# Kernel optimization log

Measured on AMD Instinct MI355X. Metric: run time of the kernel, lower is better.

## Reference

```python
import jax, jax.numpy as jnp
from jax import lax
import numpy as np

# Straight-through-estimator sign (standard BNN binarization):
# fwd: sign(x) with sign(0)=+1; bwd: pass gradient where |x|<=1 (hardtanh STE).
@jax.custom_vjp
def sign_ste(x):
    return jnp.where(x >= 0, 1.0, -1.0).astype(x.dtype)

def _sign_fwd(x):
    return sign_ste(x), x

def _sign_bwd(x, g):
    return (g * (jnp.abs(x) <= 1.0).astype(g.dtype),)

sign_ste.defvjp(_sign_fwd, _sign_bwd)

EPS = 1e-5  # BatchNorm eps (torch default)

def bn4(x, g, b):  # BatchNorm2d, training-mode batch stats, x: [N,C,H,W]
    m = x.mean((0, 2, 3), keepdims=True)
    v = x.var((0, 2, 3), keepdims=True)
    return g[None, :, None, None] * (x - m) * lax.rsqrt(v + EPS) + b[None, :, None, None]

def bn1(x, g, b):  # BatchNorm1d, x: [N,C]
    m = x.mean(0, keepdims=True)
    v = x.var(0, keepdims=True)
    return g * (x - m) * lax.rsqrt(v + EPS) + b

def bconv(x, W, b, first):
    # BinarizedConv2d: binarize weights always; binarize input except first layer.
    xb = x if first else sign_ste(x)
    y = lax.conv_general_dilated(xb, sign_ste(W), (1, 1), [(1, 1), (1, 1)],
                                 dimension_numbers=('NCHW', 'OIHW', 'NCHW'))
    return y + b[None, :, None, None]

def maxpool2(x):
    return lax.reduce_window(x, -jnp.inf, lax.max, (1, 1, 2, 2), (1, 1, 2, 2), 'VALID')

def ht(x):  # Hardtanh
    return jnp.clip(x, -1.0, 1.0)

CONV_CH = [(3, 64), (64, 128), (128, 256), (256, 256), (256, 512), (512, 512), (512, 512), (512, 512)]
LIN_CH = [(512, 512), (512, 512), (512, 10)]
POOL_AFTER = (0, 1, 3, 5, 7)  # conv indices followed by MaxPool2d

def setup_inputs():
    key = jax.random.key(0)
    ks = iter(jax.random.split(key, 64))
    d = {"x": jax.random.normal(next(ks), (256, 3, 32, 32), jnp.float32)}
    for i, (ci, co) in enumerate(CONV_CH):
        d[f"cw{i}"] = jax.random.normal(next(ks), (co, ci, 3, 3), jnp.float32) * 0.1
        d[f"cb{i}"] = jnp.zeros((co,), jnp.float32)
        d[f"cg{i}"] = jnp.ones((co,), jnp.float32)
        d[f"ct{i}"] = jnp.zeros((co,), jnp.float32)
    for i, (ci, co) in enumerate(LIN_CH):
        d[f"lw{i}"] = jax.random.normal(next(ks), (co, ci), jnp.float32) * 0.1
        d[f"lb{i}"] = jnp.zeros((co,), jnp.float32)
        d[f"lg{i}"] = jnp.ones((co,), jnp.float32)
        d[f"lt{i}"] = jnp.zeros((co,), jnp.float32)
    return d

def _forward(x, cw, cb, cg, ct, lw, lb, lg, lt):
    h = x
    for i in range(8):
        h = bconv(h, cw[i], cb[i], i == 0)
        if i in POOL_AFTER:
            h = maxpool2(h)
        h = ht(bn4(h, cg[i], ct[i]))
    h = h.reshape(h.shape[0], -1)  # [N, 512] after 5 pools on 32x32
    for i in range(3):
        h = sign_ste(h) @ sign_ste(lw[i]).T + lb[i]  # BinarizedLinear
        h = bn1(h, lg[i], lt[i])
        if i < 2:
            h = ht(h)  # Dropout is identity in eval mode
    return jax.nn.log_softmax(h, axis=-1)

def reference(x,
              cw0, cb0, cg0, ct0, cw1, cb1, cg1, ct1, cw2, cb2, cg2, ct2,
              cw3, cb3, cg3, ct3, cw4, cb4, cg4, ct4, cw5, cb5, cg5, ct5,
              cw6, cb6, cg6, ct6, cw7, cb7, cg7, ct7,
              lw0, lb0, lg0, lt0, lw1, lb1, lg1, lt1, lw2, lb2, lg2, lt2):
    cw = [cw0, cw1, cw2, cw3, cw4, cw5, cw6, cw7]
    cb = [cb0, cb1, cb2, cb3, cb4, cb5, cb6, cb7]
    cg = [cg0, cg1, cg2, cg3, cg4, cg5, cg6, cg7]
    ct = [ct0, ct1, ct2, ct3, ct4, ct5, ct6, ct7]
    lw = [lw0, lw1, lw2]
    lb = [lb0, lb1, lb2]
    lg = [lg0, lg1, lg2]
    lt = [lt0, lt1, lt2]
    return _forward(x, cw, cb, cg, ct, lw, lb, lg, lt)
```

## Files before the change

### kernel.cpp

```cpp
#include <hip/hip_runtime.h>
#include <hip/hip_bf16.h>

typedef unsigned long long u64;

#define EPSV 1e-5

__device__ __forceinline__ int imax(int a, int b) { return a > b ? a : b; }
__device__ __forceinline__ int iclamp(int v, int lo, int hi) { return v < lo ? lo : (v > hi ? hi : v); }

struct PrepArgs {
    const float* src[10];
    u64* dst[10];
    int CW[10];
    int Co[10];
    int taps[10];
    int rowbase[11];
    u64* accs;
    int naccs;
};

__global__ __launch_bounds__(256) void prep_kernel(PrepArgs a) {
    __shared__ float buf[4608];
    const int blk = blockIdx.x;
    int z = blk * 19 + threadIdx.x;
    if (threadIdx.x < 19 && z < a.naccs) a.accs[z] = 0ULL;

    int l = 0;
    while (l < 9 && blk >= a.rowbase[l + 1]) ++l;
    const int row = blk - a.rowbase[l];
    const int CW = a.CW[l];
    const int taps = a.taps[l];
    const int nf = CW * 64 * taps;
    const float* srow = a.src[l] + (size_t)row * nf;
    for (int i = threadIdx.x; i < nf; i += 256) buf[i] = srow[i];
    __syncthreads();
    const int t = threadIdx.x;
    if (t < taps * CW) {
        u64 bits = 0;
        if (taps == 9) {
            int k = t % 9, w = t / 9;
            for (int j = 0; j < 64; ++j) bits |= (u64)(buf[(w * 64 + j) * 9 + k] >= 0.f) << j;
            a.dst[l][(size_t)(k * CW + w) * a.Co[l] + row] = bits;
        } else {
            for (int j = 0; j < 64; ++j) bits |= (u64)(buf[t * 64 + j] >= 0.f) << j;
            a.dst[l][(size_t)row * CW + t] = bits;
        }
    }
}

__global__ __launch_bounds__(256) void conv0_lane(const float* __restrict__ x,
                                                  const float* __restrict__ wgt,
                                                  float* __restrict__ out,
                                                  double* __restrict__ dacc) {
    const int lane = threadIdx.x & 63;
    const int wave = threadIdx.x >> 6;
    float ws[27];
#pragma unroll
    for (int j = 0; j < 27; ++j) ws[j] = (wgt[lane * 27 + j] >= 0.f) ? 1.f : -1.f;

    const int gp0 = blockIdx.x * 32;
    const int n = gp0 >> 8;
    const int ypA = (gp0 >> 4) & 15;
    const int yb = 2 * ypA - 1;

    __shared__ float simg[3][6][34];
    const float* xb = x + (size_t)n * 3072;
    for (int t = threadIdx.x; t < 612; t += 256) {
        int ci = t / 204;
        int rem = t % 204;
        int r = rem / 34;
        int cc = rem % 34;
        int yy = yb + r;
        int xx = cc - 1;
        float v = 0.f;
        if ((unsigned)yy < 32u && (unsigned)xx < 32u) v = xb[(ci * 32 + yy) * 32 + xx];
        simg[ci][r][cc] = v;
    }
    __syncthreads();

    double s1 = 0.0, s2 = 0.0;
#pragma unroll 2
    for (int pi = 0; pi < 8; ++pi) {
        const int lp = wave * 8 + pi;
        const int gp = gp0 + lp;
        const int xp = lp & 15;
        const int rbase = 2 * (lp >> 4);
        const int cbase = 2 * xp;
        float win[3][4][4];
#pragma unroll
        for (int ci = 0; ci < 3; ++ci)
#pragma unroll
            for (int r = 0; r < 4; ++r)
#pragma unroll
                for (int c = 0; c < 4; ++c) win[ci][r][c] = simg[ci][rbase + r][cbase + c];
        float a00 = 0.f, a01 = 0.f, a10 = 0.f, a11 = 0.f;
#pragma unroll
        for (int ci = 0; ci < 3; ++ci)
#pragma unroll
            for (int ky = 0; ky < 3; ++ky)
#pragma unroll
                for (int kx = 0; kx < 3; ++kx) {
                    float wv = ws[ci * 9 + ky * 3 + kx];
                    a00 += win[ci][ky][kx] * wv;
                    a01 += win[ci][ky][kx + 1] * wv;
                    a10 += win[ci][ky + 1][kx] * wv;
                    a11 += win[ci][ky + 1][kx + 1] * wv;
                }
        float val = fmaxf(fmaxf(a00, a01), fmaxf(a10, a11));
        out[(size_t)gp * 64 + lane] = val;
        s1 += (double)val;
        s2 += (double)val * (double)val;
    }
    __shared__ double sh1[4][64], sh2[4][64];
    sh1[wave][lane] = s1;
    sh2[wave][lane] = s2;
    __syncthreads();
    if (threadIdx.x < 64) {
        double t1 = 0.0, t2 = 0.0;
#pragma unroll
        for (int r = 0; r < 4; ++r) { t1 += sh1[r][threadIdx.x]; t2 += sh2[r][threadIdx.x]; }
        double* sh = dacc + (size_t)(blockIdx.x & 7) * 1024;
        atomicAdd(&sh[2 * threadIdx.x], t1);
        atomicAdd(&sh[2 * threadIdx.x + 1], t2);
    }
}

__global__ __launch_bounds__(256) void bnpack_f(const float* __restrict__ in,
                                                const double* __restrict__ dacc,
                                                const float* __restrict__ g,
                                                const float* __restrict__ b,
                                                u64* __restrict__ act, int count) {
    __shared__ float2 sthr[64];
    if (threadIdx.x < 64) {
        int i = threadIdx.x;
        double S1 = 0.0, S2 = 0.0;
#pragma unroll
        for (int s = 0; s < 8; ++s) {
            S1 += dacc[s * 1024 + 2 * i];
            S2 += dacc[s * 1024 + 2 * i + 1];
        }
        double m = S1 / count;
        double var = S2 / count - m * m;
        double sc = (double)g[i] / sqrt(var + EPSV);
        float2 r;
        if (sc == 0.0) r = make_float2(b[i] >= 0.f ? -3.0e38f : 3.0e38f, 1.f);
        else {
            double t = m - (double)b[i] / sc;
            r = make_float2((float)t, sc > 0.0 ? 1.f : -1.f);
        }
        sthr[i] = r;
    }
    __syncthreads();
    int tid = blockIdx.x * 256 + threadIdx.x;
    int part = tid & 3;
    int word = tid >> 2;
    const float4* r4 = (const float4*)(in + (size_t)word * 64 + part * 16);
    u64 bits = 0;
#pragma unroll
    for (int q = 0; q < 4; ++q) {
        float4 v = r4[q];
        float vv[4] = {v.x, v.y, v.z, v.w};
#pragma unroll
        for (int u = 0; u < 4; ++u) {
            int c = part * 16 + q * 4 + u;
            float2 t = sthr[c];
            bool bit = (t.y > 0.f) ? (vv[u] >= t.x) : (vv[u] <= t.x);
            bits |= (u64)bit << c;
        }
    }
    bits |= __shfl_xor(bits, 1);
    bits |= __shfl_xor(bits, 2);
    if (part == 0) act[word] = bits;
}

__global__ __launch_bounds__(256) void bnpack_i(const short* __restrict__ in,
                                                const u64* __restrict__ iacc,
                                                const float* __restrict__ g,
                                                const float* __restrict__ b,
                                                u64* __restrict__ act, int Co, int wshift,
                                                int count) {
    __shared__ int2 sthr[520];
    for (int i = threadIdx.x; i < Co; i += 256) {
        long long S1 = 0, S2 = 0;
#pragma unroll
        for (int s = 0; s < 8; ++s) {
            S1 += (long long)iacc[s * 1024 + 2 * i];
            S2 += (long long)iacc[s * 1024 + 2 * i + 1];
        }
        double m = (double)S1 / count;
        double var = (double)S2 / count - m * m;
        double sc = (double)g[i] / sqrt(var + EPSV);
        int2 r;
        if (sc == 0.0) r = make_int2(b[i] >= 0.f ? (int)0x80000000 : 0x7fffffff, 0);
        else {
            double t = m - (double)b[i] / sc;
            if (t > 1.0e9) t = 1.0e9;
            if (t < -1.0e9) t = -1.0e9;
            r = (sc > 0.0) ? make_int2((int)ceil(t), 0) : make_int2((int)floor(t), 1);
        }
        sthr[(i >> 6) * 65 + (i & 63)] = r;
    }
    __syncthreads();
    int tid = blockIdx.x * 256 + threadIdx.x;
    int part = tid & 3;
    int word = tid >> 2;
    int w = word & ((1 << wshift) - 1);
    int pix = word >> wshift;
    const int4* r4 = (const int4*)(in + (size_t)pix * Co + (w << 6) + part * 16);
    u64 bits = 0;
#pragma unroll
    for (int q = 0; q < 2; ++q) {
        int4 v = r4[q];
        int words4[4] = {v.x, v.y, v.z, v.w};
#pragma unroll
        for (int u = 0; u < 4; ++u) {
#pragma unroll
            for (int h = 0; h < 2; ++h) {
                int c = part * 16 + q * 8 + u * 2 + h;
                int val = (int)(short)((h == 0) ? (words4[u] & 0xffff) : ((unsigned)words4[u] >> 16));
                int2 t = sthr[w * 65 + c];
                bool bit = t.y ? (val <= t.x) : (val >= t.x);
                bits |= (u64)bit << c;
            }
        }
    }
    bits |= __shfl_xor(bits, 1);
    bits |= __shfl_xor(bits, 2);
    if (part == 0) act[word] = bits;
}

template <int CW, int HIN, bool POOL, int WC, bool INTERIOR>
__device__ __forceinline__ void row_accum(const u64* __restrict__ inb,
                                          const u64* __restrict__ wpkT, int Co, int co,
                                          const int* yoff, const bool* ry, int* cnt) {
    constexpr int HP = POOL ? HIN / 2 : HIN;
    constexpr int WS = POOL ? 4 : 3;
    constexpr int NA = POOL ? 4 : 1;
#pragma unroll 1
    for (int w0 = 0; w0 < CW; w0 += WC) {
        u64 wg[9 * WC];
#pragma unroll
        for (int k = 0; k < 9; ++k)
#pragma unroll
            for (int w = 0; w < WC; ++w)
                wg[k * WC + w] = wpkT[(size_t)(k * CW + w0 + w) * Co + co];
        u64 cur[WS][WS][WC];
#pragma unroll
        for (int d = 0; d < WS; ++d) {
            int cc = d - 1;
            int ccc = cc < 0 ? 0 : cc;
#pragma unroll
            for (int r = 0; r < WS; ++r) {
                const u64* p = inb + yoff[r] + ccc * CW + w0;
                if (WC == 1) {
                    cur[r][d][0] = p[0];
                } else {
                    ulonglong2 v = *(const ulonglong2*)p;
                    cur[r][d][0] = v.x;
                    cur[r][d][1] = v.y;
                }
            }
        }
#pragma unroll
        for (int xp = 0; xp < HP; ++xp) {
            if constexpr (POOL) {
#pragma unroll
                for (int py = 0; py < 2; ++py)
#pragma unroll
                    for (int qx = 0; qx < 2; ++qx)
#pragma unroll
                        for (int ky = 0; ky < 3; ++ky)
#pragma unroll
                            for (int kx = 0; kx < 3; ++kx) {
                                int d = qx + kx;
                                int cc = 2 * xp + d - 1;
                                if (cc >= 0 && cc < HIN) {
#pragma unroll
                                    for (int w = 0; w < WC; ++w) {
                                        int pc = (int)__popcll(cur[py + ky][d][w] ^
                                                               wg[(ky * 3 + kx) * WC + w]);
                                        if constexpr (INTERIOR)
                                            cnt[xp * NA + py * 2 + qx] += pc;
                                        else
                                            cnt[xp * NA + py * 2 + qx] += ry[py + ky] ? pc : 0;
                                    }
                                }
                            }
            } else {
#pragma unroll
                for (int ky = 0; ky < 3; ++ky)
#pragma unroll
                    for (int kx = 0; kx < 3; ++kx) {
                        int cc = xp + kx - 1;
                        if (cc >= 0 && cc < HIN) {
#pragma unroll
                            for (int w = 0; w < WC; ++w) {
                                int pc = (int)__popcll(cur[ky][kx][w] ^
                                                       wg[(ky * 3 + kx) * WC + w]);
                                if constexpr (INTERIOR)
                                    cnt[xp] += pc;
                                else
                                    cnt[xp] += ry[ky] ? pc : 0;
                            }
                        }
                    }
            }
            if (xp < HP - 1) {
                if constexpr (POOL) {
#pragma unroll
                    for (int r = 0; r < WS; ++r)
#pragma unroll
                        for (int w = 0; w < WC; ++w) {
                            cur[r][0][w] = cur[r][2][w];
                            cur[r][1][w] = cur[r][3][w];
                        }
#pragma unroll
                    for (int dd = 2; dd < 4; ++dd) {
                        int cc = 2 * (xp + 1) + dd - 1;
                        int ccc = cc >= HIN ? HIN - 1 : cc;
#pragma unroll
                        for (int r = 0; r < WS; ++r) {
                            const u64* p = inb + yoff[r] + ccc * CW + w0;
                            if (WC == 1) {
                                cur[r][dd][0] = p[0];
                            } else {
                                ulonglong2 v = *(const ulonglong2*)p;
                                cur[r][dd][0] = v.x;
                                cur[r][dd][1] = v.y;
                            }
                        }
                    }
                } else {
#pragma unroll
                    for (int r = 0; r < WS; ++r)
#pragma unroll
                        for (int w = 0; w < WC; ++w) {
                            cur[r][0][w] = cur[r][1][w];
                            cur[r][1][w] = cur[r][2][w];
                        }
                    int cc = xp + 2;
                    int ccc = cc >= HIN ? HIN - 1 : cc;
#pragma unroll
                    for (int r = 0; r < WS; ++r) {
                        const u64* p = inb + yoff[r] + ccc * CW + w0;
                        if (WC == 1) {
                            cur[r][2][0] = p[0];
                        } else {
                            ulonglong2 v = *(const ulonglong2*)p;
                            cur[r][2][0] = v.x;
                            cur[r][2][1] = v.y;
                        }
                    }
                }
            }
        }
    }
}

template <int CW, int HIN, bool POOL, int WC>
__global__ __launch_bounds__(256) void bconv_row(const u64* __restrict__ in,
                                                 const u64* __restrict__ wpkT,
                                                 short* __restrict__ out,
                                                 u64* __restrict__ iacc, int Co) {
    constexpr int HP = POOL ? HIN / 2 : HIN;
    constexpr int WS = POOL ? 4 : 3;
    constexpr int NA = POOL ? 4 : 1;
    const int lane = threadIdx.x & 63;
    const int co = blockIdx.y * 64 + lane;
    const int grow = blockIdx.x * 4 + (threadIdx.x >> 6);
    const int n = grow / HP;
    const int yp = grow % HP;
    const int y0 = (POOL ? 2 * yp : yp) - 1;
    const u64* inb = in + (size_t)n * (HIN * HIN * CW);
    int yoff[WS];
    bool ry[WS];
#pragma unroll
    for (int r = 0; r < WS; ++r) {
        int y = y0 + r;
        ry[r] = (unsigned)y < (unsigned)HIN;
        int yc = iclamp(y, 0, HIN - 1);
        yoff[r] = yc * HIN * CW;
    }
    int cnt[HP * NA];
#pragma unroll
    for (int i = 0; i < HP * NA; ++i) cnt[i] = 0;

    if (yp > 0 && yp < HP - 1)
        row_accum<CW, HIN, POOL, WC, true>(inb, wpkT, Co, co, yoff, ry, cnt);
    else
        row_accum<CW, HIN, POOL, WC, false>(inb, wpkT, Co, co, yoff, ry, cnt);

    const int nr0 = (int)ry[0] + (int)ry[1] + (int)ry[2];
    const int nr1 = POOL ? ((int)ry[1] + (int)ry[2] + (int)ry[WS - 1]) : 0;

    int s1 = 0;
    long long s2 = 0;
    short* orow = out + (size_t)grow * HP * Co + co;
#pragma unroll
    for (int xp = 0; xp < HP; ++xp) {
        int ival;
        if constexpr (POOL) {
            int best = -2147483647;
#pragma unroll
            for (int py = 0; py < 2; ++py) {
                const int nrv = py ? nr1 : nr0;
#pragma unroll
                for (int qx = 0; qx < 2; ++qx) {
                    int ncols = 3;
                    if (xp == 0 && qx == 0) ncols = 2;
                    if (xp == HP - 1 && qx == 1) ncols = 2;
                    int v = 64 * CW * nrv * ncols - 2 * cnt[xp * NA + py * 2 + qx];
                    best = imax(best, v);
                }
            }
            ival = best;
        } else {
            const int ncols = (xp == 0 || xp == HIN - 1) ? 2 : 3;
            ival = 64 * CW * nr0 * ncols - 2 * cnt[xp];
        }
        orow[(size_t)xp * Co] = (short)ival;
        s1 += ival;
        s2 += (long long)ival * ival;
    }

    __shared__ u64 sacc[128];
    if (threadIdx.x < 128) sacc[threadIdx.x] = 0ULL;
    __syncthreads();
    atomicAdd(&sacc[lane], (u64)(long long)s1);
    atomicAdd(&sacc[64 + lane], (u64)s2);
    __syncthreads();
    u64* sh = iacc + (size_t)(blockIdx.x & 7) * 1024;
    if (threadIdx.x < 64)
        atomicAdd(&sh[2 * (blockIdx.y * 64 + threadIdx.x)], sacc[threadIdx.x]);
    else if (threadIdx.x < 128)
        atomicAdd(&sh[2 * (blockIdx.y * 64 + threadIdx.x - 64) + 1], sacc[threadIdx.x]);
}

template <int CW, int HIN, bool POOL>
__global__ __launch_bounds__(256) void bconv_tiny(const u64* __restrict__ in,
                                                  const u64* __restrict__ wpkT,
                                                  short* __restrict__ out,
                                                  u64* __restrict__ iacc, int Co) {
    constexpr int NPX = HIN * HIN;
    constexpr int HP = POOL ? HIN / 2 : HIN;
    const int lane = threadIdx.x & 63;
    const int co = blockIdx.y * 64 + lane;
    const int n = blockIdx.x * 4 + (threadIdx.x >> 6);
    const u64* inb = in + (size_t)n * CW * NPX;
    int cnt[NPX];
#pragma unroll
    for (int i = 0; i < NPX; ++i) cnt[i] = 0;

#pragma unroll 2
    for (int w = 0; w < CW; ++w) {
        u64 win[NPX];
#pragma unroll
        for (int i = 0; i < NPX; ++i) win[i] = inb[i * CW + w];
#pragma unroll
        for (int k = 0; k < 9; ++k) {
            u64 wb = wpkT[(size_t)(k * CW + w) * Co + co];
            const int ky = k / 3, kx = k % 3;
#pragma unroll
            for (int py = 0; py < HIN; ++py)
#pragma unroll
                for (int px = 0; px < HIN; ++px) {
                    const int yy = py + ky - 1, xx = px + kx - 1;
                    if (yy >= 0 && yy < HIN && xx >= 0 && xx < HIN)
                        cnt[py * HIN + px] += (int)__popcll(win[yy * HIN + xx] ^ wb);
                }
        }
    }

    int fin[NPX];
#pragma unroll
    for (int py = 0; py < HIN; ++py)
#pragma unroll
        for (int px = 0; px < HIN; ++px) {
            const int nk = ((py == 0 || py == HIN - 1) ? 2 : 3) *
                           ((px == 0 || px == HIN - 1) ? 2 : 3);
            fin[py * HIN + px] = 64 * CW * nk - 2 * cnt[py * HIN + px];
        }

    short vals[HP * HP];
    if constexpr (POOL) {
#pragma unroll
        for (int py = 0; py < HP; ++py)
#pragma unroll
            for (int px = 0; px < HP; ++px)
                vals[py * HP + px] = (short)imax(
                    imax(fin[(2 * py) * HIN + 2 * px], fin[(2 * py) * HIN + 2 * px + 1]),
                    imax(fin[(2 * py + 1) * HIN + 2 * px], fin[(2 * py + 1) * HIN + 2 * px + 1]));
    } else {
#pragma unroll
        for (int i = 0; i < NPX; ++i) vals[i] = (short)fin[i];
    }
#pragma unroll
    for (int p = 0; p < HP * HP; ++p) out[(size_t)(n * HP * HP + p) * Co + co] = vals[p];

    long long s1 = 0, s2 = 0;
#pragma unroll
    for (int p = 0; p < HP * HP; ++p) {
        s1 += vals[p];
        s2 += (long long)vals[p] * vals[p];
    }
    __shared__ u64 sacc[128];
    if (threadIdx.x < 128) sacc[threadIdx.x] = 0ULL;
    __syncthreads();
    atomicAdd(&sacc[lane], (u64)s1);
    atomicAdd(&sacc[64 + lane], (u64)s2);
    __syncthreads();
    u64* sh = iacc + (size_t)(blockIdx.x & 7) * 1024;
    if (threadIdx.x < 64)
        atomicAdd(&sh[2 * (blockIdx.y * 64 + threadIdx.x)], sacc[threadIdx.x]);
    else if (threadIdx.x < 128)
        atomicAdd(&sh[2 * (blockIdx.y * 64 + threadIdx.x - 64) + 1], sacc[threadIdx.x]);
}

__global__ __launch_bounds__(256) void lin_kernel(const u64* __restrict__ hp,
                                                  const u64* __restrict__ wp,
                                                  const float* __restrict__ lb,
                                                  const float* __restrict__ g,
                                                  const float* __restrict__ bta,
                                                  u64* __restrict__ op) {
    int o = blockIdx.x;
    int n = threadIdx.x;
    const u64* hr = hp + n * 8;
    const u64* wr = wp + o * 8;
    int s = 0;
#pragma unroll
    for (int w = 0; w < 8; ++w) s += (int)__popcll(hr[w] ^ wr[w]);
    float val = (float)(512 - 2 * s) + lb[o];
    __shared__ double sh1[256], sh2[256];
    sh1[n] = (double)val;
    sh2[n] = (double)val * (double)val;
    __syncthreads();
    for (int st = 128; st > 0; st >>= 1) {
        if (n < st) {
            sh1[n] += sh1[n + st];
            sh2[n] += sh2[n + st];
        }
        __syncthreads();
    }
    __shared__ float sm, siv;
    if (n == 0) {
        double m = sh1[0] / 256.0;
        double var = sh2[0] / 256.0 - m * m;
        sm = (float)m;
        siv = (float)(1.0 / sqrt(var + EPSV));
    }
    __syncthreads();
    float zz = g[o] * (val - sm) * siv + bta[o];
    if (zz >= 0.f) atomicOr(&op[(size_t)n * 8 + (o >> 6)], 1ULL << (o & 63));
}

__global__ __launch_bounds__(256) void lin2_lsm(const u64* __restrict__ hp,
                                                const u64* __restrict__ wp,
                                                const float* __restrict__ lb,
                                                const float* __restrict__ g,
                                                const float* __restrict__ bta,
                                                float* __restrict__ out) {
    const int n = threadIdx.x;
    const int lane = n & 63;
    const int wave = n >> 6;
    u64 h[8];
#pragma unroll
    for (int w = 0; w < 8; ++w) h[w] = hp[n * 8 + w];
    float v[10];
#pragma unroll
    for (int o = 0; o < 10; ++o) {
        int s = 0;
#pragma unroll
        for (int w = 0; w < 8; ++w) s += (int)__popcll(h[w] ^ wp[o * 8 + w]);
        v[o] = (float)(512 - 2 * s) + lb[o];
    }
    __shared__ double w1[4][10], w2[4][10];
#pragma unroll
    for (int o = 0; o < 10; ++o) {
        double a = (double)v[o];
        double b = a * a;
#pragma unroll
        for (int off = 32; off > 0; off >>= 1) {
            a += __shfl_xor(a, off);
            b += __shfl_xor(b, off);
        }
        if (lane == 0) {
            w1[wave][o] = a;
            w2[wave][o] = b;
        }
    }
    __syncthreads();
    float z[10];
#pragma unroll
    for (int o = 0; o < 10; ++o) {
        double S1 = w1[0][o] + w1[1][o] + w1[2][o] + w1[3][o];
        double S2 = w2[0][o] + w2[1][o] + w2[2][o] + w2[3][o];
        double m = S1 / 256.0;
        double var = S2 / 256.0 - m * m;
        float sm = (float)m;
        float siv = (float)(1.0 / sqrt(var + EPSV));
        z[o] = g[o] * (v[o] - sm) * siv + bta[o];
    }
    float mx = z[0];
#pragma unroll
    for (int o = 1; o < 10; ++o) mx = fmaxf(mx, z[o]);
    float se = 0.f;
#pragma unroll
    for (int o = 0; o < 10; ++o) se += expf(z[o] - mx);
    float ls = logf(se);
#pragma unroll
    for (int o = 0; o < 10; ++o) out[n * 10 + o] = z[o] - mx - ls;
}

extern "C" void kernel_launch(void* const* d_in, const int* in_sizes, int n_in, void* d_out,
                              int out_size, void* d_ws, size_t ws_size, hipStream_t stream) {
    (void)in_sizes; (void)n_in; (void)out_size; (void)ws_size;
    const float* x = (const float*)d_in[0];
    const float *cw[8], *cb[8], *cg[8], *ct[8];
    for (int i = 0; i < 8; ++i) {
        cw[i] = (const float*)d_in[1 + 4 * i];
        cb[i] = (const float*)d_in[2 + 4 * i];
        cg[i] = (const float*)d_in[3 + 4 * i];
        ct[i] = (const float*)d_in[4 + 4 * i];
    }
    const float *lw[3], *lb[3], *lg[3], *lt[3];
    for (int i = 0; i < 3; ++i) {
        lw[i] = (const float*)d_in[33 + 4 * i];
        lb[i] = (const float*)d_in[34 + 4 * i];
        lg[i] = (const float*)d_in[35 + 4 * i];
        lt[i] = (const float*)d_in[36 + 4 * i];
    }

    static const int CIs[8] = {3, 64, 128, 256, 256, 512, 512, 512};
    static const int COs[8] = {64, 128, 256, 256, 512, 512, 512, 512};
    static const int HPs[8] = {16, 8, 8, 4, 4, 2, 2, 1};

    char* ws = (char*)d_ws;
    size_t off = 0;
    auto alloc = [&](size_t bytes) -> void* {
        void* p = ws + off;
        off += (bytes + 255) & ~(size_t)255;
        return p;
    };

    u64* accs = (u64*)alloc((size_t)8 * 8 * 1024 * 8);
    u64* fcs0 = (u64*)alloc(2048 * 8);
    u64* fcs1 = (u64*)alloc(2048 * 8);
    double* dacc0 = (double*)accs;
    auto iacc = [&](int layer) { return accs + (size_t)layer * 8192; };

    u64* wpkT[8] = {};
    for (int i = 1; i < 8; ++i) wpkT[i] = (u64*)alloc((size_t)COs[i] * 9 * (CIs[i] / 64) * 8);
    u64* wpl[3];
    int LO[3] = {512, 512, 10};
    for (int i = 0; i < 3; ++i) wpl[i] = (u64*)alloc((size_t)LO[i] * 8 * 8);
    u64* act[8];
    for (int i = 0; i < 8; ++i) act[i] = (u64*)alloc((size_t)256 * (COs[i] / 64) * HPs[i] * HPs[i] * 8);
    float* out0 = (float*)alloc((size_t)65536 * 64 * 4);
    short* i16A = (short*)alloc((size_t)16384 * 256 * 2);
    short* i16B = (short*)alloc((size_t)16384 * 256 * 2);

    PrepArgs pa;
    int rb = 0;
    for (int i = 1; i < 8; ++i) {
        int e = i - 1;
        pa.src[e] = cw[i];
        pa.dst[e] = wpkT[i];
        pa.CW[e] = CIs[i] / 64;
        pa.Co[e] = COs[i];
        pa.taps[e] = 9;
        pa.rowbase[e] = rb;
        rb += COs[i];
    }
    for (int i = 0; i < 3; ++i) {
        int e = 7 + i;
        pa.src[e] = lw[i];
        pa.dst[e] = wpl[i];
        pa.CW[e] = 8;
        pa.Co[e] = LO[i];
        pa.taps[e] = 1;
        pa.rowbase[e] = rb;
        rb += LO[i];
    }
    pa.rowbase[10] = rb;
    pa.accs = accs;
    pa.naccs = 8 * 8 * 1024 + 2048 + 2048;
    prep_kernel<<<rb, 256, 0, stream>>>(pa);

    conv0_lane<<<2048, 256, 0, stream>>>(x, cw[0], out0, dacc0);
    bnpack_f<<<1024, 256, 0, stream>>>(out0, dacc0, cg[0], ct[0], act[0], 65536);

    bconv_row<1, 16, true, 1><<<dim3(512, 2), 256, 0, stream>>>(act[0], wpkT[1], i16A, iacc(1), 128);
    bnpack_i<<<512, 256, 0, stream>>>(i16A, iacc(1), cg[1], ct[1], act[1], 128, 1, 16384);

    bconv_row<2, 8, false, 2><<<dim3(512, 4), 256, 0, stream>>>(act[1], wpkT[2], i16B, iacc(2), 256);
    bnpack_i<<<1024, 256, 0, stream>>>(i16B, iacc(2), cg[2], ct[2], act[2], 256, 2, 16384);

    bconv_row<4, 8, true, 2><<<dim3(256, 4), 256, 0, stream>>>(act[2], wpkT[3], i16A, iacc(3), 256);
    bnpack_i<<<256, 256, 0, stream>>>(i16A, iacc(3), cg[3], ct[3], act[3], 256, 2, 4096);

    bconv_row<4, 4, false, 2><<<dim3(256, 8), 256, 0, stream>>>(act[3], wpkT[4], i16B, iacc(4), 512);
    bnpack_i<<<512, 256, 0, stream>>>(i16B, iacc(4), cg[4], ct[4], act[4], 512, 3, 4096);

    bconv_tiny<8, 4, true><<<dim3(64, 8), 256, 0, stream>>>(act[4], wpkT[5], i16A, iacc(5), 512);
    bnpack_i<<<128, 256, 0, stream>>>(i16A, iacc(5), cg[5], ct[5], act[5], 512, 3, 1024);

    bconv_tiny<8, 2, false><<<dim3(64, 8), 256, 0, stream>>>(act[5], wpkT[6], i16B, iacc(6), 512);
    bnpack_i<<<128, 256, 0, stream>>>(i16B, iacc(6), cg[6], ct[6], act[6], 512, 3, 1024);

    bconv_tiny<8, 2, true><<<dim3(64, 8), 256, 0, stream>>>(act[6], wpkT[7], i16A, iacc(7), 512);
    bnpack_i<<<32, 256, 0, stream>>>(i16A, iacc(7), cg[7], ct[7], act[7], 512, 3, 256);

    lin_kernel<<<512, 256, 0, stream>>>(act[7], wpl[0], lb[0], lg[0], lt[0], fcs0);
    lin_kernel<<<512, 256, 0, stream>>>(fcs0, wpl[1], lb[1], lg[1], lt[1], fcs1);
    lin2_lsm<<<1, 256, 0, stream>>>(fcs1, wpl[2], lb[2], lg[2], lt[2], (float*)d_out);
}
```

Before: 421.9 us.

## Fuse BN-threshold bit-packing into consumer conv kernels via shared-memory staging

Removes the separate bnpack kernels between conv layers. Each conv kernel now computes the previous layer's BN thresholds itself, binarizes the int16/float activations for its needed input rows into shared memory, and convolves from LDS. This eliminates seven kernel launches and the packed-activation round trip through global memory. In exchange, every block redundantly recomputes the thresholds, and halo rows are re-binarized by neighbouring blocks.

```diff
diff --git a/kernel.cpp b/kernel.cpp
--- a/kernel.cpp
+++ b/kernel.cpp
@@ -125,54 +125,6 @@
     }
 }
 
-__global__ __launch_bounds__(256) void bnpack_f(const float* __restrict__ in,
-                                                const double* __restrict__ dacc,
-                                                const float* __restrict__ g,
-                                                const float* __restrict__ b,
-                                                u64* __restrict__ act, int count) {
-    __shared__ float2 sthr[64];
-    if (threadIdx.x < 64) {
-        int i = threadIdx.x;
-        double S1 = 0.0, S2 = 0.0;
-#pragma unroll
-        for (int s = 0; s < 8; ++s) {
-            S1 += dacc[s * 1024 + 2 * i];
-            S2 += dacc[s * 1024 + 2 * i + 1];
-        }
-        double m = S1 / count;
-        double var = S2 / count - m * m;
-        double sc = (double)g[i] / sqrt(var + EPSV);
-        float2 r;
-        if (sc == 0.0) r = make_float2(b[i] >= 0.f ? -3.0e38f : 3.0e38f, 1.f);
-        else {
-            double t = m - (double)b[i] / sc;
-            r = make_float2((float)t, sc > 0.0 ? 1.f : -1.f);
-        }
-        sthr[i] = r;
-    }
-    __syncthreads();
-    int tid = blockIdx.x * 256 + threadIdx.x;
-    int part = tid & 3;
-    int word = tid >> 2;
-    const float4* r4 = (const float4*)(in + (size_t)word * 64 + part * 16);
-    u64 bits = 0;
-#pragma unroll
-    for (int q = 0; q < 4; ++q) {
-        float4 v = r4[q];
-        float vv[4] = {v.x, v.y, v.z, v.w};
-#pragma unroll
-        for (int u = 0; u < 4; ++u) {
-            int c = part * 16 + q * 4 + u;
-            float2 t = sthr[c];
-            bool bit = (t.y > 0.f) ? (vv[u] >= t.x) : (vv[u] <= t.x);
-            bits |= (u64)bit << c;
-        }
-    }
-    bits |= __shfl_xor(bits, 1);
-    bits |= __shfl_xor(bits, 2);
-    if (part == 0) act[word] = bits;
-}
-
 __global__ __launch_bounds__(256) void bnpack_i(const short* __restrict__ in,
                                                 const u64* __restrict__ iacc,
                                                 const float* __restrict__ g,
@@ -357,21 +309,137 @@
     }
 }
 
-template <int CW, int HIN, bool POOL, int WC>
-__global__ __launch_bounds__(256) void bconv_row(const u64* __restrict__ in,
-                                                 const u64* __restrict__ wpkT,
-                                                 short* __restrict__ out,
-                                                 u64* __restrict__ iacc, int Co) {
+template <int CW, int HIN, bool POOL, int WC, bool FIRST>
+__global__ __launch_bounds__(256) void bconv_row_f(const void* __restrict__ inprev,
+                                                   const void* __restrict__ pstats,
+                                                   const float* __restrict__ pg,
+                                                   const float* __restrict__ pb, int pcount,
+                                                   const u64* __restrict__ wpkT,
+                                                   short* __restrict__ out,
+                                                   u64* __restrict__ iacc, int Co) {
     constexpr int HP = POOL ? HIN / 2 : HIN;
     constexpr int WS = POOL ? 4 : 3;
     constexpr int NA = POOL ? 4 : 1;
+    constexpr int ROWS = POOL ? 10 : 6;
+    constexpr int Ci = CW * 64;
+    __shared__ __align__(16) u64 sU[ROWS * HIN * CW];
+    __shared__ int2 sthr[CW * 65];
+    __shared__ float2 sthf[64];
+
+    if constexpr (FIRST) {
+        if (threadIdx.x < 64) {
+            const double* dacc = (const double*)pstats;
+            int i = threadIdx.x;
+            double S1 = 0.0, S2 = 0.0;
+#pragma unroll
+            for (int s = 0; s < 8; ++s) {
+                S1 += dacc[s * 1024 + 2 * i];
+                S2 += dacc[s * 1024 + 2 * i + 1];
+            }
+            double m = S1 / pcount;
+            double var = S2 / pcount - m * m;
+            double sc = (double)pg[i] / sqrt(var + EPSV);
+            float2 r;
+            if (sc == 0.0) r = make_float2(pb[i] >= 0.f ? -3.0e38f : 3.0e38f, 1.f);
+            else {
+                double t = m - (double)pb[i] / sc;
+                r = make_float2((float)t, sc > 0.0 ? 1.f : -1.f);
+            }
+            sthf[i] = r;
+        }
+    } else {
+        const u64* pacc = (const u64*)pstats;
+        for (int i = threadIdx.x; i < Ci; i += 256) {
+            long long S1 = 0, S2 = 0;
+#pragma unroll
+            for (int s = 0; s < 8; ++s) {
+                S1 += (long long)pacc[s * 1024 + 2 * i];
+                S2 += (long long)pacc[s * 1024 + 2 * i + 1];
+            }
+            double m = (double)S1 / pcount;
+            double var = (double)S2 / pcount - m * m;
+            double sc = (double)pg[i] / sqrt(var + EPSV);
+            int2 r;
+            if (sc == 0.0) r = make_int2(pb[i] >= 0.f ? (int)0x80000000 : 0x7fffffff, 0);
+            else {
+                double t = m - (double)pb[i] / sc;
+                if (t > 1.0e9) t = 1.0e9;
+                if (t < -1.0e9) t = -1.0e9;
+                r = (sc > 0.0) ? make_int2((int)ceil(t), 0) : make_int2((int)floor(t), 1);
+            }
+            sthr[(i >> 6) * 65 + (i & 63)] = r;
+        }
+    }
+    __syncthreads();
+
+    const int bi = blockIdx.x;
+    constexpr int BPN = HP / 4;
+    const int n = bi / BPN;
+    const int yp0 = (bi % BPN) * 4;
+    const int ylo = imax(0, (POOL ? 2 * yp0 : yp0) - 1);
+    const int yhiU = POOL ? (2 * yp0 + 8) : (yp0 + 4);
+    const int yhi = yhiU > HIN - 1 ? HIN - 1 : yhiU;
+    const int nrows = yhi - ylo + 1;
+    const int nw = nrows * HIN * CW;
+
+    if constexpr (FIRST) {
+        const float* src = (const float*)inprev;
+        for (int t = threadIdx.x; t < nw; t += 256) {
+            int x = t % HIN;
+            int yr = t / HIN;
+            int y = ylo + yr;
+            const float4* p = (const float4*)(src + (size_t)((n * 16 + y) * 16 + x) * 64);
+            u64 bits = 0;
+#pragma unroll
+            for (int q = 0; q < 16; ++q) {
+                float4 v = p[q];
+                float vv[4] = {v.x, v.y, v.z, v.w};
+#pragma unroll
+                for (int u = 0; u < 4; ++u) {
+                    int c = q * 4 + u;
+                    float2 th = sthf[c];
+                    bool bit = (th.y > 0.f) ? (vv[u] >= th.x) : (vv[u] <= th.x);
+                    bits |= (u64)bit << c;
+                }
+            }
+            sU[t] = bits;
+        }
+    } else {
+        const short* src = (const short*)inprev;
+        for (int t = threadIdx.x; t < nw; t += 256) {
+            int w = t % CW;
+            int x = (t / CW) % HIN;
+            int yr = t / (HIN * CW);
+            int y = ylo + yr;
+            const int4* p = (const int4*)(src + (size_t)((n * HIN + y) * HIN + x) * Ci + w * 64);
+            u64 bits = 0;
+#pragma unroll
+            for (int q = 0; q < 8; ++q) {
+                int4 v = p[q];
+                int wd[4] = {v.x, v.y, v.z, v.w};
+#pragma unroll
+                for (int u = 0; u < 4; ++u) {
+#pragma unroll
+                    for (int h = 0; h < 2; ++h) {
+                        int j = q * 8 + u * 2 + h;
+                        int val = (int)(short)((h == 0) ? (wd[u] & 0xffff) : ((unsigned)wd[u] >> 16));
+                        int2 th = sthr[w * 65 + j];
+                        bool bit = th.y ? (val <= th.x) : (val >= th.x);
+                        bits |= (u64)bit << j;
+                    }
+                }
+            }
+            sU[t] = bits;
+        }
+    }
+    __syncthreads();
+
     const int lane = threadIdx.x & 63;
+    const int wave = threadIdx.x >> 6;
     const int co = blockIdx.y * 64 + lane;
-    const int grow = blockIdx.x * 4 + (threadIdx.x >> 6);
-    const int n = grow / HP;
-    const int yp = grow % HP;
+    const int yp = yp0 + wave;
+    const int grow = n * HP + yp;
     const int y0 = (POOL ? 2 * yp : yp) - 1;
-    const u64* inb = in + (size_t)n * (HIN * HIN * CW);
     int yoff[WS];
     bool ry[WS];
 #pragma unroll
@@ -379,16 +447,16 @@
         int y = y0 + r;
         ry[r] = (unsigned)y < (unsigned)HIN;
         int yc = iclamp(y, 0, HIN - 1);
-        yoff[r] = yc * HIN * CW;
+        yoff[r] = (yc - ylo) * (HIN * CW);
     }
     int cnt[HP * NA];
 #pragma unroll
     for (int i = 0; i < HP * NA; ++i) cnt[i] = 0;
 
     if (yp > 0 && yp < HP - 1)
-        row_accum<CW, HIN, POOL, WC, true>(inb, wpkT, Co, co, yoff, ry, cnt);
+        row_accum<CW, HIN, POOL, WC, true>(sU, wpkT, Co, co, yoff, ry, cnt);
     else
-        row_accum<CW, HIN, POOL, WC, false>(inb, wpkT, Co, co, yoff, ry, cnt);
+        row_accum<CW, HIN, POOL, WC, false>(sU, wpkT, Co, co, yoff, ry, cnt);
 
     const int nr0 = (int)ry[0] + (int)ry[1] + (int)ry[2];
     const int nr1 = POOL ? ((int)ry[1] + (int)ry[2] + (int)ry[WS - 1]) : 0;
@@ -437,16 +505,73 @@
 }
 
 template <int CW, int HIN, bool POOL>
-__global__ __launch_bounds__(256) void bconv_tiny(const u64* __restrict__ in,
-                                                  const u64* __restrict__ wpkT,
-                                                  short* __restrict__ out,
-                                                  u64* __restrict__ iacc, int Co) {
+__global__ __launch_bounds__(256) void bconv_tiny_f(const short* __restrict__ inprev,
+                                                    const u64* __restrict__ pacc,
+                                                    const float* __restrict__ pg,
+                                                    const float* __restrict__ pb, int pcount,
+                                                    const u64* __restrict__ wpkT,
+                                                    short* __restrict__ out,
+                                                    u64* __restrict__ iacc, int Co) {
     constexpr int NPX = HIN * HIN;
     constexpr int HP = POOL ? HIN / 2 : HIN;
+    constexpr int Ci = CW * 64;
+    __shared__ int2 sthr[CW * 65];
+    __shared__ u64 sU[4][NPX * CW];
+
+    for (int i = threadIdx.x; i < Ci; i += 256) {
+        long long S1 = 0, S2 = 0;
+#pragma unroll
+        for (int s = 0; s < 8; ++s) {
+            S1 += (long long)pacc[s * 1024 + 2 * i];
+            S2 += (long long)pacc[s * 1024 + 2 * i + 1];
+        }
+        double m = (double)S1 / pcount;
+        double var = (double)S2 / pcount - m * m;
+        double sc = (double)pg[i] / sqrt(var + EPSV);
+        int2 r;
+        if (sc == 0.0) r = make_int2(pb[i] >= 0.f ? (int)0x80000000 : 0x7fffffff, 0);
+        else {
+            double t = m - (double)pb[i] / sc;
+            if (t > 1.0e9) t = 1.0e9;
+            if (t < -1.0e9) t = -1.0e9;
+            r = (sc > 0.0) ? make_int2((int)ceil(t), 0) : make_int2((int)floor(t), 1);
+        }
+        sthr[(i >> 6) * 65 + (i & 63)] = r;
+    }
+    __syncthreads();
+
+    const int nbase = blockIdx.x * 4;
+    for (int t = threadIdx.x; t < 4 * NPX * CW; t += 256) {
+        int img = t / (NPX * CW);
+        int rem = t % (NPX * CW);
+        int w = rem % CW;
+        int i = rem / CW;
+        const int4* p = (const int4*)(inprev + (size_t)((nbase + img) * NPX + i) * Ci + w * 64);
+        u64 bits = 0;
+#pragma unroll
+        for (int q = 0; q < 8; ++q) {
+            int4 v = p[q];
+            int wd[4] = {v.x, v.y, v.z, v.w};
+#pragma unroll
+            for (int u = 0; u < 4; ++u) {
+#pragma unroll
+                for (int h = 0; h < 2; ++h) {
+                    int j = q * 8 + u * 2 + h;
+                    int val = (int)(short)((h == 0) ? (wd[u] & 0xffff) : ((unsigned)wd[u] >> 16));
+                    int2 th = sthr[w * 65 + j];
+                    bool bit = th.y ? (val <= th.x) : (val >= th.x);
+                    bits |= (u64)bit << j;
+                }
+            }
+        }
+        sU[img][i * CW + w] = bits;
+    }
+    __syncthreads();
+
     const int lane = threadIdx.x & 63;
     const int co = blockIdx.y * 64 + lane;
-    const int n = blockIdx.x * 4 + (threadIdx.x >> 6);
-    const u64* inb = in + (size_t)n * CW * NPX;
+    const int n = nbase + (threadIdx.x >> 6);
+    const u64* inb = sU[threadIdx.x >> 6];
     int cnt[NPX];
 #pragma unroll
     for (int i = 0; i < NPX; ++i) cnt[i] = 0;
@@ -632,7 +757,6 @@
 
     static const int CIs[8] = {3, 64, 128, 256, 256, 512, 512, 512};
     static const int COs[8] = {64, 128, 256, 256, 512, 512, 512, 512};
-    static const int HPs[8] = {16, 8, 8, 4, 4, 2, 2, 1};
 
     char* ws = (char*)d_ws;
     size_t off = 0;
@@ -653,8 +777,7 @@
     u64* wpl[3];
     int LO[3] = {512, 512, 10};
     for (int i = 0; i < 3; ++i) wpl[i] = (u64*)alloc((size_t)LO[i] * 8 * 8);
-    u64* act[8];
-    for (int i = 0; i < 8; ++i) act[i] = (u64*)alloc((size_t)256 * (COs[i] / 64) * HPs[i] * HPs[i] * 8);
+    u64* act7 = (u64*)alloc((size_t)256 * 8 * 8);
     float* out0 = (float*)alloc((size_t)65536 * 64 * 4);
     short* i16A = (short*)alloc((size_t)16384 * 256 * 2);
     short* i16B = (short*)alloc((size_t)16384 * 256 * 2);
@@ -687,30 +810,31 @@
     prep_kernel<<<rb, 256, 0, stream>>>(pa);
 
     conv0_lane<<<2048, 256, 0, stream>>>(x, cw[0], out0, dacc0);
-    bnpack_f<<<1024, 256, 0, stream>>>(out0, dacc0, cg[0], ct[0], act[0], 65536);
-
-    bconv_row<1, 16, true, 1><<<dim3(512, 2), 256, 0, stream>>>(act[0], wpkT[1], i16A, iacc(1), 128);
-    bnpack_i<<<512, 256, 0, stream>>>(i16A, iacc(1), cg[1], ct[1], act[1], 128, 1, 16384);
-
-    bconv_row<2, 8, false, 2><<<dim3(512, 4), 256, 0, stream>>>(act[1], wpkT[2], i16B, iacc(2), 256);
-    bnpack_i<<<1024, 256, 0, stream>>>(i16B, iacc(2), cg[2], ct[2], act[2], 256, 2, 16384);
-
-    bconv_row<4, 8, true, 2><<<dim3(256, 4), 256, 0, stream>>>(act[2], wpkT[3], i16A, iacc(3), 256);
-    bnpack_i<<<256, 256, 0, stream>>>(i16A, iacc(3), cg[3], ct[3], act[3], 256, 2, 4096);
-
-    bconv_row<4, 4, false, 2><<<dim3(256, 8), 256, 0, stream>>>(act[3], wpkT[4], i16B, iacc(4), 512);
-    bnpack_i<<<512, 256, 0, stream>>>(i16B, iacc(4), cg[4], ct[4], act[4], 512, 3, 4096);
-
-    bconv_tiny<8, 4, true><<<dim3(64, 8), 256, 0, stream>>>(act[4], wpkT[5], i16A, iacc(5), 512);
-    bnpack_i<<<128, 256, 0, stream>>>(i16A, iacc(5), cg[5], ct[5], act[5], 512, 3, 1024);
-
-    bconv_tiny<8, 2, false><<<dim3(64, 8), 256, 0, stream>>>(act[5], wpkT[6], i16B, iacc(6), 512);
-    bnpack_i<<<128, 256, 0, stream>>>(i16B, iacc(6), cg[6], ct[6], act[6], 512, 3, 1024);
-
-    bconv_tiny<8, 2, true><<<dim3(64, 8), 256, 0, stream>>>(act[6], wpkT[7], i16A, iacc(7), 512);
-    bnpack_i<<<32, 256, 0, stream>>>(i16A, iacc(7), cg[7], ct[7], act[7], 512, 3, 256);
-
-    lin_kernel<<<512, 256, 0, stream>>>(act[7], wpl[0], lb[0], lg[0], lt[0], fcs0);
+
+    bconv_row_f<1, 16, true, 1, true><<<dim3(512, 2), 256, 0, stream>>>(
+        out0, dacc0, cg[0], ct[0], 65536, wpkT[1], i16A, iacc(1), 128);
+
+    bconv_row_f<2, 8, false, 2, false><<<dim3(512, 4), 256, 0, stream>>>(
+        i16A, iacc(1), cg[1], ct[1], 16384, wpkT[2], i16B, iacc(2), 256);
+
+    bconv_row_f<4, 8, true, 2, false><<<dim3(256, 4), 256, 0, stream>>>(
+        i16B, iacc(2), cg[2], ct[2], 16384, wpkT[3], i16A, iacc(3), 256);
+
+    bconv_row_f<4, 4, false, 2, false><<<dim3(256, 8), 256, 0, stream>>>(
+        i16A, iacc(3), cg[3], ct[3], 4096, wpkT[4], i16B, iacc(4), 512);
+
+    bconv_tiny_f<8, 4, true><<<dim3(64, 8), 256, 0, stream>>>(
+        i16B, iacc(4), cg[4], ct[4], 4096, wpkT[5], i16A, iacc(5), 512);
+
+    bconv_tiny_f<8, 2, false><<<dim3(64, 8), 256, 0, stream>>>(
+        i16A, iacc(5), cg[5], ct[5], 1024, wpkT[6], i16B, iacc(6), 512);
+
+    bconv_tiny_f<8, 2, true><<<dim3(64, 8), 256, 0, stream>>>(
+        i16B, iacc(6), cg[6], ct[6], 1024, wpkT[7], i16A, iacc(7), 512);
+
+    bnpack_i<<<32, 256, 0, stream>>>(i16A, iacc(7), cg[7], ct[7], act7, 512, 3, 256);
+
+    lin_kernel<<<512, 256, 0, stream>>>(act7, wpl[0], lb[0], lg[0], lt[0], fcs0);
     lin_kernel<<<512, 256, 0, stream>>>(fcs0, wpl[1], lb[1], lg[1], lt[1], fcs1);
     lin2_lsm<<<1, 256, 0, stream>>>(fcs1, wpl[2], lb[2], lg[2], lt[2], (float*)d_out);
 }
```

After: 405.9 us. -3.8%, faster.
